# Kernel tuning notes

Measured on AMD Instinct MI355X. Metric: run time of the kernel, lower is better.

## Reference

```python
import jax, jax.numpy as jnp
import numpy as np

NUM_HEADS = 16

def setup_inputs() -> dict:
    key = jax.random.key(0)
    k1, k2, k3 = jax.random.split(key, 3)
    B, T, C = 2, 2048, 1024
    x = jax.random.normal(k1, (B, T, C), dtype=jnp.float32)
    w_qkv = jax.random.normal(k2, (3 * C, C), dtype=jnp.float32) * (C ** -0.5)
    w_out = jax.random.normal(k3, (C, C), dtype=jnp.float32) * (C ** -0.5)
    b_out = jnp.zeros((C,), dtype=jnp.float32)
    return {"x": x, "w_qkv": w_qkv, "w_out": w_out, "b_out": b_out}

def reference(x, w_qkv, w_out, b_out):
    B, T, C = x.shape
    H = NUM_HEADS
    dh = C // H
    scale = 1.0 / jnp.sqrt(jnp.float32(dh))
    # fused qkv projection (torch Linear: x @ W^T), no bias
    qkv = jnp.einsum('btc,dc->btd', x, w_qkv)  # [B,T,3C]
    q, k, v = jnp.split(qkv, 3, axis=-1)
    # [B,H,T,dh]
    q = q.reshape(B, T, H, dh).transpose(0, 2, 1, 3)
    k = k.reshape(B, T, H, dh).transpose(0, 2, 1, 3)
    v = v.reshape(B, T, H, dh).transpose(0, 2, 1, 3)
    att = jnp.einsum('bhqd,bhkd->bhqk', q, k) * scale  # [B,H,T,T]
    causal = jnp.tril(jnp.ones((T, T), dtype=bool))
    att = jnp.where(causal[None, None, :, :], att, jnp.float32(-jnp.inf))
    att = jax.nn.softmax(att, axis=-1)
    y = jnp.einsum('bhqk,bhkd->bhqd', att, v)  # [B,H,T,dh]
    y = y.transpose(0, 2, 1, 3).reshape(B, T, C)
    y = jnp.einsum('btc,dc->btd', y, w_out) + b_out
    return y
```

## Files before the change

kernel.cpp:

```cpp
#include <hip/hip_runtime.h>
#include <hip/hip_bf16.h>
#include <math.h>

typedef __bf16 bf16x8 __attribute__((ext_vector_type(8)));
typedef __bf16 bf16x4 __attribute__((ext_vector_type(4)));
typedef float  f32x4  __attribute__((ext_vector_type(4)));

#define MFMA16(A, B, C) __builtin_amdgcn_mfma_f32_16x16x32_bf16(A, B, C, 0, 0, 0)

__device__ __forceinline__ void gload_lds16(const void* g, void* l) {
  __builtin_amdgcn_global_load_lds((const __attribute__((address_space(1))) void*)g,
                                   (__attribute__((address_space(3))) void*)l, 16, 0, 0);
}

__device__ __forceinline__ float exp2_fast(float x) {
  float r; asm("v_exp_f32 %0, %1" : "=v"(r) : "v"(x)); return r;
}

__device__ __forceinline__ unsigned lds_off(const void* p) {
  return (unsigned)(size_t)(const __attribute__((address_space(3))) void*)p;
}

__device__ __forceinline__ bf16x4 ds_tr16(unsigned byte_addr) {
  bf16x4 r;
  asm volatile("ds_read_b64_tr_b16 %0, %1" : "=v"(r) : "v"(byte_addr));
  return r;
}

__global__ __launch_bounds__(256) void cvt_all(const float* __restrict__ x,
                                               const float* __restrict__ wq,
                                               const float* __restrict__ wo,
                                               __bf16* __restrict__ xb,
                                               __bf16* __restrict__ wqb,
                                               __bf16* __restrict__ wob) {
  int i = (blockIdx.x * 256 + threadIdx.x) * 8;
  const float* s;
  __bf16*      d;
  if (i < 4194304) {
    s = x; d = xb;
  } else if (i < 4194304 + 3145728) {
    i -= 4194304; s = wq; d = wqb;
  } else {
    i -= 4194304 + 3145728; s = wo; d = wob;
  }
  const float4 a = *(const float4*)(s + i);
  const float4 b = *(const float4*)(s + i + 4);
  bf16x8 v;
  v[0] = (__bf16)a.x; v[1] = (__bf16)a.y; v[2] = (__bf16)a.z; v[3] = (__bf16)a.w;
  v[4] = (__bf16)b.x; v[5] = (__bf16)b.y; v[6] = (__bf16)b.z; v[7] = (__bf16)b.w;
  *(bf16x8*)(d + i) = v;
}

template <bool BIAS, typename CT>
__global__ __launch_bounds__(256) void gemm_bt64(const __bf16* __restrict__ A,
                                                 const __bf16* __restrict__ B,
                                                 const float* __restrict__ bias,
                                                 CT* __restrict__ C, int M, int N,
                                                 int K) {
  __shared__ alignas(16) __bf16 As[2][64 * 32];
  __shared__ alignas(16) __bf16 Bs[2][128 * 32];

  const int tid  = threadIdx.x;
  const int lane = tid & 63;
  const int ql   = lane & 15;
  const int g    = lane >> 4;
  const int wv   = tid >> 6;
  const int row0 = blockIdx.y * 64;
  const int col0 = blockIdx.x * 128;
  const int NT   = K >> 5;

  f32x4 acc[4][2] = {};

  auto stage = [&](int buf, int kt) {
    const int k0 = kt << 5;
    {
      const int row  = tid >> 2;
      const int slot = (tid & 3) ^ ((row >> 1) & 3);
      gload_lds16(A + (size_t)(row0 + row) * K + (k0 + slot * 8), &As[buf][wv * 512]);
    }
#pragma unroll
    for (int i = 0; i < 2; ++i) {
      const int n    = i * 256 + tid;
      const int row  = n >> 2;
      const int slot = (n & 3) ^ ((row >> 1) & 3);
      gload_lds16(B + (size_t)(col0 + row) * K + (k0 + slot * 8),
                  &Bs[buf][(i * 256 + wv * 64) * 8]);
    }
  };

  stage(0, 0);
  __syncthreads();
  int cur = 0;
  for (int kt = 0; kt < NT; ++kt) {
    if (kt + 1 < NT) stage(cur ^ 1, kt + 1);

    bf16x8 af[4], bfr[2];
#pragma unroll
    for (int m = 0; m < 4; ++m) {
      const int row  = m * 16 + ql;
      const int slot = g ^ ((row >> 1) & 3);
      af[m] = *(const bf16x8*)&As[cur][row * 32 + slot * 8];
    }
#pragma unroll
    for (int n = 0; n < 2; ++n) {
      const int row  = wv * 32 + n * 16 + ql;
      const int slot = g ^ ((row >> 1) & 3);
      bfr[n] = *(const bf16x8*)&Bs[cur][row * 32 + slot * 8];
    }
#pragma unroll
    for (int m = 0; m < 4; ++m)
#pragma unroll
      for (int n = 0; n < 2; ++n) acc[m][n] = MFMA16(af[m], bfr[n], acc[m][n]);

    __syncthreads();
    cur ^= 1;
  }

#pragma unroll
  for (int n = 0; n < 2; ++n) {
    const int   col = col0 + wv * 32 + n * 16 + ql;
    const float bv  = BIAS ? bias[col] : 0.0f;
#pragma unroll
    for (int m = 0; m < 4; ++m) {
      const int rbase = row0 + m * 16 + (g << 2);
#pragma unroll
      for (int r = 0; r < 4; ++r)
        C[(size_t)(rbase + r) * N + col] = (CT)(acc[m][n][r] + bv);
    }
  }
}

__global__ __launch_bounds__(256) void attn_fwd(const __bf16* __restrict__ qkv,
                                                __bf16* __restrict__ yo) {
  __shared__ alignas(16) __bf16 Ks[2][64 * 64];
  __shared__ alignas(16) __bf16 Vs[2][64 * 64];

  const int tid  = threadIdx.x;
  const int lane = tid & 63;
  const int ql   = lane & 15;
  const int g    = lane >> 4;
  const int wv   = tid >> 6;

  const int bid = blockIdx.x;
  const int qt  = 31 - (bid >> 5);
  const int bh  = bid & 31;
  const int b   = bh >> 4;
  const int h   = bh & 15;
  const int q0  = qt * 64;
  const int qw  = q0 + wv * 16;
  const int NT  = qt + 1;

  const size_t  rs = 3072;
  const __bf16* Qg = qkv + (size_t)b * 2048 * rs + h * 64;
  const __bf16* Kg = Qg + 1024;
  const __bf16* Vg = Qg + 2048;

  const int slotK = ((tid & 7) ^ ((tid >> 3) & 7)) << 3;
  const int keyV  = ((tid >> 5) << 2) + ((tid >> 1) & 3);
  const int dV    = (((tid >> 3) & 3) << 4) + ((tid & 1) << 3);
  const __bf16* kP0 = Kg + (size_t)(tid >> 3) * rs + slotK;
  const __bf16* kP1 = kP0 + 32 * rs;
  const __bf16* vP0 = Vg + (size_t)keyV * rs + dV;
  const __bf16* vP1 = vP0 + 32 * rs;
  const size_t  step = 64 * rs;

  auto stageKV = [&](int buf) {
    gload_lds16(kP0, &Ks[buf][wv * 512]);
    gload_lds16(kP1, &Ks[buf][2048 + wv * 512]);
    gload_lds16(vP0, &Vs[buf][wv * 512]);
    gload_lds16(vP1, &Vs[buf][2048 + wv * 512]);
    kP0 += step; kP1 += step; vP0 += step; vP1 += step;
  };

  bf16x8 aQ[2];
#pragma unroll
  for (int ks = 0; ks < 2; ++ks) {
    aQ[ks] = *(const bf16x8*)(Qg + (size_t)(qw + ql) * rs + ks * 32 + (g << 3));
#pragma unroll
    for (int e = 0; e < 8; ++e) aQ[ks][e] = aQ[ks][e] * (__bf16)0.125f;
  }

  bf16x8 vones;
#pragma unroll
  for (int e = 0; e < 8; ++e) vones[e] = (__bf16)1.0f;

  f32x4 o[5] = {};

  const float L = 1.44269504088896f;
  const unsigned vbase = lds_off(&Vs[0][0]);

  int cur = 0;
  stageKV(0);
  __syncthreads();

  for (int t = 0; t < NT; ++t) {
    const int  k0  = t << 6;
    const bool pre = (t + 1 < NT);
    if (pre) stageKV(cur ^ 1);

    f32x4 sc[4] = {};
    __builtin_amdgcn_s_setprio(1);
#pragma unroll
    for (int n = 0; n < 4; ++n) {
#pragma unroll
      for (int ks = 0; ks < 2; ++ks) {
        const int krow = n * 16 + ql;
        const int slot = ((ks << 2) + g) ^ (krow & 7);
        bf16x8    kf   = *(const bf16x8*)&Ks[cur][krow * 64 + slot * 8];
        sc[n]          = MFMA16(kf, aQ[ks], sc[n]);
      }
    }
    __builtin_amdgcn_s_setprio(0);

    const unsigned abase = vbase + (cur ? 8192u : 0u) + (g << 10) + (ql << 3);
    bf16x4 vlo[2][4], vhi[2][4];
#pragma unroll
    for (int ks = 0; ks < 2; ++ks)
#pragma unroll
      for (int n = 0; n < 4; ++n) {
        vlo[ks][n] = ds_tr16(abase + ks * 4096 + n * 128);
        vhi[ks][n] = ds_tr16(abase + ks * 4096 + n * 128 + 512);
      }

    float s16[4][4];
    if (t == NT - 1) {
      const int q = qw + ql;
#pragma unroll
      for (int n = 0; n < 4; ++n)
#pragma unroll
        for (int r = 0; r < 4; ++r) {
          const int k = k0 + n * 16 + (g << 2) + r;
          s16[n][r]   = (k > q) ? -INFINITY : sc[n][r];
        }
    } else {
#pragma unroll
      for (int n = 0; n < 4; ++n)
#pragma unroll
        for (int r = 0; r < 4; ++r) s16[n][r] = sc[n][r];
    }

    int W[8];
#pragma unroll
    for (int n = 0; n < 4; ++n)
#pragma unroll
      for (int rp = 0; rp < 2; ++rp) {
        union { __bf16 hh[2]; int i; } pk;
        pk.hh[0]      = (__bf16)exp2_fast(s16[n][2 * rp] * L);
        pk.hh[1]      = (__bf16)exp2_fast(s16[n][2 * rp + 1] * L);
        W[2 * n + rp] = pk.i;
      }

    union { int w[4]; bf16x8 v; } pa[2];
#pragma unroll
    for (int ks = 0; ks < 2; ++ks) {
      int a0 = W[4 * ks + 0], b0 = W[4 * ks + 2];
      asm("v_permlane32_swap_b32 %0, %1" : "+v"(a0), "+v"(b0));
      asm("v_permlane16_swap_b32 %0, %1" : "+v"(a0), "+v"(b0));
      pa[ks].w[0] = a0;
      pa[ks].w[2] = b0;
      int a1 = W[4 * ks + 1], b1 = W[4 * ks + 3];
      asm("v_permlane32_swap_b32 %0, %1" : "+v"(a1), "+v"(b1));
      asm("v_permlane16_swap_b32 %0, %1" : "+v"(a1), "+v"(b1));
      pa[ks].w[1] = a1;
      pa[ks].w[3] = b1;
    }

    asm volatile("s_waitcnt lgkmcnt(0)");
    __builtin_amdgcn_sched_barrier(0);

    __builtin_amdgcn_s_setprio(1);
#pragma unroll
    for (int ks = 0; ks < 2; ++ks) {
#pragma unroll
      for (int n = 0; n < 4; ++n) {
        bf16x8 vf;
#pragma unroll
        for (int e = 0; e < 4; ++e) { vf[e] = vlo[ks][n][e]; vf[e + 4] = vhi[ks][n][e]; }
        o[n] = MFMA16(pa[ks].v, vf, o[n]);
      }
      o[4] = MFMA16(pa[ks].v, vones, o[4]);
    }
    __builtin_amdgcn_s_setprio(0);

    __syncthreads();
    cur ^= 1;
  }

#pragma unroll
  for (int n = 0; n < 4; ++n) {
    const int d = n * 16 + ql;
#pragma unroll
    for (int r = 0; r < 4; ++r) {
      const int q = qw + (g << 2) + r;
      yo[((size_t)b * 2048 + q) * 1024 + h * 64 + d] = (__bf16)(o[n][r] / o[4][r]);
    }
  }
}

extern "C" void kernel_launch(void* const* d_in, const int* in_sizes, int n_in, void* d_out,
                              int out_size, void* d_ws, size_t ws_size, hipStream_t stream) {
  (void)in_sizes; (void)n_in; (void)out_size; (void)ws_size;
  const float* x     = (const float*)d_in[0];
  const float* w_qkv = (const float*)d_in[1];
  const float* w_out = (const float*)d_in[2];
  const float* b_out = (const float*)d_in[3];
  float*       out   = (float*)d_out;

  __bf16* xb    = (__bf16*)d_ws;
  __bf16* wqkvb = xb + (size_t)4096 * 1024;
  __bf16* woutb = wqkvb + (size_t)3072 * 1024;
  __bf16* qkv   = woutb + (size_t)1024 * 1024;
  __bf16* yatt  = qkv + (size_t)4096 * 3072;

  cvt_all<<<4096, 256, 0, stream>>>(x, w_qkv, w_out, xb, wqkvb, woutb);

  gemm_bt64<false, __bf16><<<dim3(24, 64), 256, 0, stream>>>(xb, wqkvb, nullptr, qkv,
                                                             4096, 3072, 1024);
  attn_fwd<<<1024, 256, 0, stream>>>(qkv, yatt);
  gemm_bt64<true, float><<<dim3(8, 64), 256, 0, stream>>>(yatt, woutb, b_out, out,
                                                          4096, 1024, 1024);
}
```

Measured before the change: 114.7 us.

## Replace QKV projection GEMM with 256x256 8-phase pipelined bf16 kernel

Adds a new 512-thread GEMM with 256x256 output tiles, K-step 64, double-buffered half-tile LDS staging via direct global-to-LDS loads, and swizzled LDS layout. The main loop is split into eight phases that interleave prefetch of the next half-tiles with MFMA work, using explicit waitcnt, barriers and priority boosts. It is used only for the QKV projection, cutting the grid to 192 blocks with far more reuse per block. The risks are reduced occupancy, tail effects from fewer blocks, and K and M hardcoded to 1024 and a multiple of 256.

```diff
diff --git a/kernel.cpp b/kernel.cpp
--- a/kernel.cpp
+++ b/kernel.cpp
@@ -51,6 +51,119 @@
   *(bf16x8*)(d + i) = v;
 }
 
+__global__ __launch_bounds__(512, 2) void gemm_8ph(const __bf16* __restrict__ A,
+                                                   const __bf16* __restrict__ B,
+                                                   __bf16* __restrict__ C, int N) {
+  __shared__ alignas(16) __bf16 LA[2][2][128 * 64];
+  __shared__ alignas(16) __bf16 LB[2][2][128 * 64];
+
+  const int tid  = threadIdx.x;
+  const int lane = tid & 63;
+  const int wv   = tid >> 6;
+  const int wr   = wv >> 2;
+  const int wc   = wv & 3;
+  const int row0 = blockIdx.y * 256;
+  const int col0 = blockIdx.x * 256;
+
+  const int srow = tid >> 3;
+  const int sswz = ((tid & 7) ^ (srow & 7)) << 3;
+
+  auto stageHalf = [&](const __bf16* mat, int base0, int tile, int h, __bf16* dst) {
+#pragma unroll
+    for (int i = 0; i < 2; ++i)
+      gload_lds16(mat + (size_t)(base0 + h * 128 + i * 64 + srow) * 1024 + tile * 64 + sswz,
+                  dst + (i * 512 + wv * 64) * 8);
+  };
+
+  f32x4  acc[8][4] = {};
+  bf16x8 bfr[4][2];
+
+  stageHalf(B, col0, 0, 0, &LB[0][0][0]);
+  stageHalf(B, col0, 0, 1, &LB[0][1][0]);
+  stageHalf(A, row0, 0, 0, &LA[0][0][0]);
+  stageHalf(A, row0, 0, 1, &LA[0][1][0]);
+  stageHalf(B, col0, 1, 0, &LB[1][0][0]);
+  stageHalf(B, col0, 1, 1, &LB[1][1][0]);
+  __builtin_amdgcn_sched_barrier(0);
+  asm volatile("s_waitcnt vmcnt(4)" ::: "memory");
+  __builtin_amdgcn_s_barrier();
+  __builtin_amdgcn_sched_barrier(0);
+
+#pragma unroll 1
+  for (int it = 0; it < 8; ++it) {
+    const int E = 2 * it;
+#pragma unroll
+    for (int q = 0; q < 8; ++q) {
+      const int P = q >> 2;
+      const int p = q & 3;
+
+      bf16x8 af[2][2];
+#pragma unroll
+      for (int mm = 0; mm < 2; ++mm) {
+        const int r = (p * 2 + mm) * 16 + (lane & 15);
+#pragma unroll
+        for (int ks = 0; ks < 2; ++ks) {
+          const int sl = ((ks << 2) + (lane >> 4)) ^ (r & 7);
+          af[mm][ks]   = *(const bf16x8*)&LA[P][wr][r * 64 + sl * 8];
+        }
+      }
+      if (p == 0) {
+#pragma unroll
+        for (int n = 0; n < 4; ++n) {
+          const int rB = (wc & 1) * 64 + n * 16 + (lane & 15);
+#pragma unroll
+          for (int ks = 0; ks < 2; ++ks) {
+            const int sl = ((ks << 2) + (lane >> 4)) ^ (rB & 7);
+            bfr[n][ks]   = *(const bf16x8*)&LB[P][wc >> 1][rB * 64 + sl * 8];
+          }
+        }
+      }
+
+      if (q == 0)      stageHalf(A, row0, E + 1, 0, &LA[1][0][0]);
+      else if (q == 1) stageHalf(A, row0, E + 1, 1, &LA[1][1][0]);
+      else if (q == 2) stageHalf(B, col0, E + 2, 0, &LB[0][0][0]);
+      else if (q == 3) stageHalf(B, col0, E + 2, 1, &LB[0][1][0]);
+      else if (q == 4) stageHalf(A, row0, E + 2, 0, &LA[0][0][0]);
+      else if (q == 5) stageHalf(A, row0, E + 2, 1, &LA[0][1][0]);
+      else if (q == 6) stageHalf(B, col0, E + 3, 0, &LB[1][0][0]);
+      else             stageHalf(B, col0, E + 3, 1, &LB[1][1][0]);
+
+      __builtin_amdgcn_sched_barrier(0);
+      __builtin_amdgcn_s_barrier();
+      asm volatile("s_waitcnt lgkmcnt(0)" ::: "memory");
+      __builtin_amdgcn_sched_barrier(0);
+
+      __builtin_amdgcn_s_setprio(1);
+#pragma unroll
+      for (int mm = 0; mm < 2; ++mm)
+#pragma unroll
+        for (int n = 0; n < 4; ++n)
+#pragma unroll
+          for (int ks = 0; ks < 2; ++ks)
+            acc[p * 2 + mm][n] = MFMA16(af[mm][ks], bfr[n][ks], acc[p * 2 + mm][n]);
+      __builtin_amdgcn_s_setprio(0);
+      __builtin_amdgcn_sched_barrier(0);
+
+      if (q == 3 || q == 7)
+        asm volatile("s_waitcnt vmcnt(4)" ::: "memory");
+      __builtin_amdgcn_s_barrier();
+      __builtin_amdgcn_sched_barrier(0);
+    }
+  }
+
+#pragma unroll
+  for (int n = 0; n < 4; ++n) {
+    const int col = col0 + wc * 64 + n * 16 + (lane & 15);
+#pragma unroll
+    for (int m = 0; m < 8; ++m) {
+      const int rbase = row0 + wr * 128 + m * 16 + ((lane >> 4) << 2);
+#pragma unroll
+      for (int r = 0; r < 4; ++r)
+        C[(size_t)(rbase + r) * N + col] = (__bf16)acc[m][n][r];
+    }
+  }
+}
+
 template <bool BIAS, typename CT>
 __global__ __launch_bounds__(256) void gemm_bt64(const __bf16* __restrict__ A,
                                                  const __bf16* __restrict__ B,
@@ -314,8 +427,7 @@
 
   cvt_all<<<4096, 256, 0, stream>>>(x, w_qkv, w_out, xb, wqkvb, woutb);
 
-  gemm_bt64<false, __bf16><<<dim3(24, 64), 256, 0, stream>>>(xb, wqkvb, nullptr, qkv,
-                                                             4096, 3072, 1024);
+  gemm_8ph<<<dim3(12, 16), 512, 0, stream>>>(xb, wqkvb, qkv, 3072);
   attn_fwd<<<1024, 256, 0, stream>>>(qkv, yatt);
   gemm_bt64<true, float><<<dim3(8, 64), 256, 0, stream>>>(yatt, woutb, b_out, out,
                                                           4096, 1024, 1024);
```

Result: faster. 101.0 us (-11.9%).
